# Kernel tuning notes

Hardware: AMD Instinct MI355X
Metric: run time of the kernel (lower is better)

## Reference

```python
import jax, jax.numpy as jnp
import numpy as np

B, D, KM1 = 8192, 256, 64  # batch, feature dim (no bias), num_classes-1
NC = KM1 + 1


def setup_inputs() -> dict:
    key = jax.random.key(0)
    k1, k2, k3 = jax.random.split(key, 3)
    features = jax.random.normal(k1, (B, D), dtype=jnp.float32)
    y = jax.random.randint(k2, (B,), 0, NC)
    mu = jax.random.normal(k3, (D, KM1), dtype=jnp.float32) * 0.001
    Sigma = jnp.broadcast_to(jnp.eye(D, dtype=jnp.float32), (KM1, D, D)).copy()
    return {"features": features, "y": y, "mu": mu, "Sigma": Sigma, "loss_type": 1}


def _b_ky(nc):
    # (nc, nc-1) stick-breaking selector matrix
    return 1.0 - jnp.pad(jnp.eye(nc)[..., :-2], [(0, 0), (1, 0)]).cumsum(-1)


def reference(features, y, mu, Sigma, loss_type):
    x = features                      # use_bias=False -> pad is a no-op
    logits = x @ mu                   # (B, K-1)
    bky = _b_ky(NC)                   # (K, K-1)
    y1h = jax.nn.one_hot(y, NC)       # (B, K)
    if loss_type == 0:
        full = jnp.pad(logits, [(0, 0), (0, 1)]) - jax.nn.softplus(logits) @ bky.T
        return -jnp.sum(full * y1h, -1)
    else:
        # psi_k = sqrt(x^T (Sigma_k + mu_k mu_k^T) x) = sqrt(x^T Sigma_k x + (x.mu_k)^2)
        xSx = jnp.einsum('bd,kde,be->bk', x, Sigma, x)   # (B, K-1)
        psi = jnp.sqrt(xSx + logits * logits)
        b = y1h @ bky                 # (B, K-1)
        kappa = y1h[..., :-1] - b / 2
        return -jnp.sum(logits * kappa + b * (psi / 2 - jax.nn.softplus(psi)), -1)
```

## Files before the change

### kernel.cpp

```cpp
#include <hip/hip_runtime.h>

typedef __attribute__((ext_vector_type(8))) short bf16x8;
typedef __attribute__((ext_vector_type(4))) float f32x4;

#define B_N 8192
#define D_N 256
#define K_N 64

__device__ __forceinline__ unsigned short bf16_rne(float f) {
  unsigned u = __builtin_bit_cast(unsigned, f);
  u += 0x7fffu + ((u >> 16) & 1u);
  return (unsigned short)(u >> 16);
}
__device__ __forceinline__ float bf16_f32(unsigned short h) {
  return __builtin_bit_cast(float, (unsigned)h << 16);
}

__device__ __forceinline__ void gload_lds16(const void* g, void* l) {
  __builtin_amdgcn_global_load_lds(
      (const __attribute__((address_space(1))) unsigned int*)g,
      (__attribute__((address_space(3))) unsigned int*)l, 16, 0, 0);
}

__global__ void convert_kernel(const float* __restrict__ src,
                               ushort* __restrict__ hi, ushort* __restrict__ lo,
                               int n4) {
  int idx = blockIdx.x * blockDim.x + threadIdx.x;
  int stride = gridDim.x * blockDim.x;
  for (int i = idx; i < n4; i += stride) {
    float4 v = ((const float4*)src)[i];
    ushort4 h, l;
    h.x = bf16_rne(v.x); l.x = bf16_rne(v.x - bf16_f32(h.x));
    h.y = bf16_rne(v.y); l.y = bf16_rne(v.y - bf16_f32(h.y));
    h.z = bf16_rne(v.z); l.z = bf16_rne(v.z - bf16_f32(h.z));
    h.w = bf16_rne(v.w); l.w = bf16_rne(v.w - bf16_f32(h.w));
    ((ushort4*)hi)[i] = h;
    ((ushort4*)lo)[i] = l;
  }
}

__global__ void convert_T_kernel(const float* __restrict__ Sigma,
                                 ushort* __restrict__ Th,
                                 ushort* __restrict__ Tl) {
  const int dtab[10] = {0, 0, 0, 0, 1, 1, 1, 2, 2, 3};
  const int etab[10] = {0, 1, 2, 3, 1, 2, 3, 2, 3, 3};
  const int k = blockIdx.x;
  const int dblk = dtab[blockIdx.y], eblk = etab[blockIdx.y];
  const float wgt = (dblk == eblk) ? 0.5f : 1.0f;
  const int tid = threadIdx.x;
  const int dl = tid >> 2;
  const int el0 = (tid & 3) * 16;
  const int d = dblk * 64 + dl;
  const size_t rowbase = ((size_t)k * D_N + d) * D_N + eblk * 64 + el0;
  const float* Srow = Sigma + rowbase;
  const float* Scol = Sigma + ((size_t)k * D_N + eblk * 64 + el0) * D_N + d;
  ushort h[16], l[16];
#pragma unroll
  for (int i = 0; i < 16; ++i) {
    const float t = (Srow[i] + Scol[(size_t)i * D_N]) * wgt;
    h[i] = bf16_rne(t);
    l[i] = bf16_rne(t - bf16_f32(h[i]));
  }
  *(uint4*)(Th + rowbase) = *(uint4*)&h[0];
  *(uint4*)(Th + rowbase + 8) = *(uint4*)&h[8];
  *(uint4*)(Tl + rowbase) = *(uint4*)&l[0];
  *(uint4*)(Tl + rowbase + 8) = *(uint4*)&l[8];
}

__global__ __launch_bounds__(256, 4) void xsx_tri2_kernel(
    const float* __restrict__ X,
    const ushort* __restrict__ Xh, const ushort* __restrict__ Xl,
    const ushort* __restrict__ Th, const ushort* __restrict__ Tl,
    float* __restrict__ part) {
  __shared__ __align__(16) ushort A_h[128][32];
  __shared__ __align__(16) ushort A_l[128][32];
  __shared__ __align__(16) ushort B_h[2][64][32];
  __shared__ __align__(16) ushort B_l[2][64][32];

  const int tid = threadIdx.x;
  const int lane = tid & 63;
  const int wid = tid >> 6;
  const int lr = lane & 15;
  const int lk = lane >> 4;

  const int bid = blockIdx.x;
  const int xcd = bid & 7;
  const int r = bid >> 3;
  const int qd = r >> 8;
  const int kp = (r >> 6) & 3;
  const int bg = r & 63;
  const int kk0 = xcd * 8 + kp * 2;
  const int bbase = bg * 128;

  const int srow = lane >> 2;
  const int sc = ((lane & 3) ^ ((lane >> 3) & 3)) * 8;
  const int rdc = (lk ^ ((lr >> 1) & 3)) * 8;

  f32x4 acc[2][2][4];
#pragma unroll
  for (int kp2 = 0; kp2 < 2; ++kp2)
#pragma unroll
    for (int mi = 0; mi < 2; ++mi)
#pragma unroll
      for (int ni = 0; ni < 4; ++ni)
        acc[kp2][mi][ni] = (f32x4){0.f, 0.f, 0.f, 0.f};

  const size_t a0 = (size_t)(bbase + wid * 32 + srow) * D_N + sc;
  const size_t bK0 = (size_t)kk0 * (D_N * D_N) +
                     (size_t)(qd * 64 + wid * 16 + srow) * D_N + sc;
  const size_t bK1 = bK0 + (size_t)(D_N * D_N);

  const int nch = 2 * (4 - qd);
  for (int c = 0; c < nch; ++c) {
    const int e0 = qd * 64 + c * 32;
    __syncthreads();
    gload_lds16(Xh + a0 + e0, &A_h[wid * 32][0]);
    gload_lds16(Xh + a0 + (size_t)16 * D_N + e0, &A_h[wid * 32 + 16][0]);
    gload_lds16(Xl + a0 + e0, &A_l[wid * 32][0]);
    gload_lds16(Xl + a0 + (size_t)16 * D_N + e0, &A_l[wid * 32 + 16][0]);
    gload_lds16(Th + bK0 + e0, &B_h[0][wid * 16][0]);
    gload_lds16(Tl + bK0 + e0, &B_l[0][wid * 16][0]);
    gload_lds16(Th + bK1 + e0, &B_h[1][wid * 16][0]);
    gload_lds16(Tl + bK1 + e0, &B_l[1][wid * 16][0]);
    __syncthreads();

    bf16x8 ah[2], al[2];
#pragma unroll
    for (int mi = 0; mi < 2; ++mi) {
      ah[mi] = *(const bf16x8*)&A_h[wid * 32 + mi * 16 + lr][rdc];
      al[mi] = *(const bf16x8*)&A_l[wid * 32 + mi * 16 + lr][rdc];
    }
#pragma unroll
    for (int kp2 = 0; kp2 < 2; ++kp2) {
#pragma unroll
      for (int ni = 0; ni < 4; ++ni) {
        const bf16x8 bh = *(const bf16x8*)&B_h[kp2][ni * 16 + lr][rdc];
        const bf16x8 bl = *(const bf16x8*)&B_l[kp2][ni * 16 + lr][rdc];
#pragma unroll
        for (int mi = 0; mi < 2; ++mi)
          acc[kp2][mi][ni] = __builtin_amdgcn_mfma_f32_16x16x32_bf16(
              ah[mi], bh, acc[kp2][mi][ni], 0, 0, 0);
#pragma unroll
        for (int mi = 0; mi < 2; ++mi)
          acc[kp2][mi][ni] = __builtin_amdgcn_mfma_f32_16x16x32_bf16(
              al[mi], bh, acc[kp2][mi][ni], 0, 0, 0);
#pragma unroll
        for (int mi = 0; mi < 2; ++mi)
          acc[kp2][mi][ni] = __builtin_amdgcn_mfma_f32_16x16x32_bf16(
              ah[mi], bl, acc[kp2][mi][ni], 0, 0, 0);
      }
    }
  }

#pragma unroll
  for (int kp2 = 0; kp2 < 2; ++kp2) {
#pragma unroll
    for (int mi = 0; mi < 2; ++mi) {
#pragma unroll
      for (int jj = 0; jj < 4; ++jj) {
        const int brow = bbase + wid * 32 + mi * 16 + lk * 4 + jj;
        const float* xr = X + (size_t)brow * D_N + qd * 64 + lr;
        float p = 0.f;
#pragma unroll
        for (int ni = 0; ni < 4; ++ni)
          p = fmaf(acc[kp2][mi][ni][jj], xr[ni * 16], p);
        p += __shfl_xor(p, 1);
        p += __shfl_xor(p, 2);
        p += __shfl_xor(p, 4);
        p += __shfl_xor(p, 8);
        if (lr == 0) part[((size_t)brow * K_N + kk0 + kp2) * 4 + qd] = p;
      }
    }
  }
}

__global__ __launch_bounds__(512, 2) void xsx_fallback(
    const float* __restrict__ X, const float* __restrict__ Sigma,
    float* __restrict__ xsx) {
  constexpr int BM = 128, KT = 32;
  __shared__ __align__(16) ushort Ah[BM][KT];
  __shared__ __align__(16) ushort Al[BM][KT];
  __shared__ __align__(16) ushort Bh[D_N][KT];
  __shared__ __align__(16) ushort Bl[D_N][KT];
  __shared__ float red[4][BM];

  const int tid = threadIdx.x;
  const int lane = tid & 63;
  const int wid = tid >> 6;
  const int wm = wid >> 2;
  const int wn = wid & 3;
  const int lr = lane & 15;
  const int lk = lane >> 4;

  const int b0 = blockIdx.x * BM;
  const int kk = blockIdx.y;
  const size_t soff = (size_t)kk * D_N * D_N;

  f32x4 acc[4][4];
#pragma unroll
  for (int mi = 0; mi < 4; ++mi)
#pragma unroll
    for (int ni = 0; ni < 4; ++ni) acc[mi][ni] = (f32x4){0.f, 0.f, 0.f, 0.f};

  for (int ec = 0; ec < D_N / KT; ++ec) {
    const int e0 = ec * KT;
    __syncthreads();
#pragma unroll
    for (int r = 0; r < 2; ++r) {
      const int i = tid + 512 * r;
      const int row = i >> 3, c4 = (i & 7) * 4;
      const float4 v = *(const float4*)(X + (size_t)(b0 + row) * D_N + e0 + c4);
      ushort4 h, l;
      h.x = bf16_rne(v.x); l.x = bf16_rne(v.x - bf16_f32(h.x));
      h.y = bf16_rne(v.y); l.y = bf16_rne(v.y - bf16_f32(h.y));
      h.z = bf16_rne(v.z); l.z = bf16_rne(v.z - bf16_f32(h.z));
      h.w = bf16_rne(v.w); l.w = bf16_rne(v.w - bf16_f32(h.w));
      *(ushort4*)&Ah[row][c4] = h;
      *(ushort4*)&Al[row][c4] = l;
    }
#pragma unroll
    for (int r = 0; r < 4; ++r) {
      const int i = tid + 512 * r;
      const int d = i >> 3, c4 = (i & 7) * 4;
      const float4 v = *(const float4*)(Sigma + soff + (size_t)d * D_N + e0 + c4);
      ushort4 h, l;
      h.x = bf16_rne(v.x); l.x = bf16_rne(v.x - bf16_f32(h.x));
      h.y = bf16_rne(v.y); l.y = bf16_rne(v.y - bf16_f32(h.y));
      h.z = bf16_rne(v.z); l.z = bf16_rne(v.z - bf16_f32(h.z));
      h.w = bf16_rne(v.w); l.w = bf16_rne(v.w - bf16_f32(h.w));
      *(ushort4*)&Bh[d][c4] = h;
      *(ushort4*)&Bl[d][c4] = l;
    }
    __syncthreads();

    bf16x8 ah[4], al[4];
#pragma unroll
    for (int mi = 0; mi < 4; ++mi) {
      ah[mi] = *(const bf16x8*)&Ah[wm * 64 + mi * 16 + lr][lk * 8];
      al[mi] = *(const bf16x8*)&Al[wm * 64 + mi * 16 + lr][lk * 8];
    }
#pragma unroll
    for (int ni = 0; ni < 4; ++ni) {
      const bf16x8 bh = *(const bf16x8*)&Bh[wn * 64 + ni * 16 + lr][lk * 8];
      const bf16x8 bl = *(const bf16x8*)&Bl[wn * 64 + ni * 16 + lr][lk * 8];
#pragma unroll
      for (int mi = 0; mi < 4; ++mi) {
        acc[mi][ni] = __builtin_amdgcn_mfma_f32_16x16x32_bf16(ah[mi], bh, acc[mi][ni], 0, 0, 0);
        acc[mi][ni] = __builtin_amdgcn_mfma_f32_16x16x32_bf16(al[mi], bh, acc[mi][ni], 0, 0, 0);
        acc[mi][ni] = __builtin_amdgcn_mfma_f32_16x16x32_bf16(ah[mi], bl, acc[mi][ni], 0, 0, 0);
      }
    }
  }

  float p[4][4];
#pragma unroll
  for (int mi = 0; mi < 4; ++mi)
#pragma unroll
    for (int jj = 0; jj < 4; ++jj) p[mi][jj] = 0.f;
#pragma unroll
  for (int mi = 0; mi < 4; ++mi) {
#pragma unroll
    for (int jj = 0; jj < 4; ++jj) {
      const int brow = b0 + wm * 64 + mi * 16 + lk * 4 + jj;
      const float* xr = X + (size_t)brow * D_N + wn * 64 + lr;
#pragma unroll
      for (int ni = 0; ni < 4; ++ni)
        p[mi][jj] = fmaf(acc[mi][ni][jj], xr[ni * 16], p[mi][jj]);
    }
  }
#pragma unroll
  for (int mi = 0; mi < 4; ++mi)
#pragma unroll
    for (int jj = 0; jj < 4; ++jj) {
      float v = p[mi][jj];
      v += __shfl_xor(v, 1);
      v += __shfl_xor(v, 2);
      v += __shfl_xor(v, 4);
      v += __shfl_xor(v, 8);
      p[mi][jj] = v;
    }
  if (lr == 0) {
#pragma unroll
    for (int mi = 0; mi < 4; ++mi)
#pragma unroll
      for (int jj = 0; jj < 4; ++jj)
        red[wn][wm * 64 + mi * 16 + lk * 4 + jj] = p[mi][jj];
  }
  __syncthreads();
  if (tid < BM) {
    const float s = red[0][tid] + red[1][tid] + red[2][tid] + red[3][tid];
    xsx[(size_t)(b0 + tid) * K_N + kk] = s;
  }
}

__global__ __launch_bounds__(256) void loss_kernel(
    const float* __restrict__ X, const int* __restrict__ y,
    const float* __restrict__ mu, const int* __restrict__ loss_type,
    const float* __restrict__ xsx, float* __restrict__ out, int nparts) {
  __shared__ float mu_s[D_N * K_N];
  __shared__ float x_s[4][D_N];
  const int tid = threadIdx.x;
  const int wid = tid >> 6;
  const int lane = tid & 63;
  const int b = blockIdx.x * 4 + wid;

  for (int i = tid; i < D_N * K_N / 4; i += 256)
    ((float4*)mu_s)[i] = ((const float4*)mu)[i];
  ((float4*)&x_s[wid][0])[lane] = ((const float4*)(X + (size_t)b * D_N))[lane];
  __syncthreads();

  const int yb = y[b];
  const int lt = loss_type[0];

  float logit = 0.f;
#pragma unroll 8
  for (int d = 0; d < D_N; ++d)
    logit = fmaf(x_s[wid][d], mu_s[d * K_N + lane], logit);

  float term;
  if (lt == 1) {
    float xv;
    if (nparts == 4) {
      const float4 pv = *(const float4*)(xsx + ((size_t)b * K_N + lane) * 4);
      xv = ((pv.x + pv.y) + pv.z) + pv.w;
    } else {
      xv = xsx[(size_t)b * K_N + lane];
    }
    const float psi = sqrtf(fmaxf(xv + logit * logit, 0.f));
    const float bk = (lane <= yb) ? 1.f : 0.f;
    const float kap = ((lane == yb) ? 1.f : 0.f) - 0.5f * bk;
    term = logit * kap + bk * (-0.5f * psi - log1pf(expf(-psi)));
  } else {
    const float sp = (logit > 0.f) ? (logit + log1pf(expf(-logit)))
                                   : log1pf(expf(logit));
    term = ((lane == yb) ? logit : 0.f) - ((lane <= yb) ? sp : 0.f);
  }
#pragma unroll
  for (int s = 1; s < 64; s <<= 1) term += __shfl_xor(term, s);
  if (lane == 0) out[b] = -term;
}

extern "C" void kernel_launch(void* const* d_in, const int* in_sizes, int n_in,
                              void* d_out, int out_size, void* d_ws, size_t ws_size,
                              hipStream_t stream) {
  const float* X = (const float*)d_in[0];
  const int* y = (const int*)d_in[1];
  const float* mu = (const float*)d_in[2];
  const float* Sigma = (const float*)d_in[3];
  const int* lt = (const int*)d_in[4];
  float* out = (float*)d_out;

  const size_t XN = (size_t)B_N * D_N;
  const size_t SN = (size_t)K_N * D_N * D_N;
  const size_t xh_off = 0;
  const size_t xl_off = xh_off + XN * 2;
  const size_t th_off = xl_off + XN * 2;
  const size_t tl_off = th_off + SN * 2;
  const size_t part_off = tl_off + SN * 2;
  const size_t need = part_off + (size_t)B_N * K_N * 4 * 4;

  char* w = (char*)d_ws;
  if (ws_size >= need) {
    ushort* Xh = (ushort*)(w + xh_off);
    ushort* Xl = (ushort*)(w + xl_off);
    ushort* Th = (ushort*)(w + th_off);
    ushort* Tl = (ushort*)(w + tl_off);
    float* part = (float*)(w + part_off);
    hipLaunchKernelGGL(convert_kernel, dim3(1024), dim3(256), 0, stream,
                       X, Xh, Xl, (int)(XN / 4));
    hipLaunchKernelGGL(convert_T_kernel, dim3(64, 10), dim3(256), 0, stream,
                       Sigma, Th, Tl);
    hipLaunchKernelGGL(xsx_tri2_kernel, dim3(8192), dim3(256), 0, stream,
                       X, Xh, Xl, Th, Tl, part);
    hipLaunchKernelGGL(loss_kernel, dim3(B_N / 4), dim3(256), 0, stream,
                       X, y, mu, lt, part, out, 4);
  } else {
    float* xsx = (float*)w;
    hipLaunchKernelGGL(xsx_fallback, dim3(B_N / 128, K_N), dim3(512), 0, stream,
                       X, Sigma, xsx);
    hipLaunchKernelGGL(loss_kernel, dim3(B_N / 4), dim3(256), 0, stream,
                       X, y, mu, lt, xsx, out, 1);
  }
}
```

Baseline: 202.1 us.

## Split xSx blocks to one class each and batch loss kernel rows per block

The xSx MFMA kernel now handles a single class k per block instead of two, which halves the B-tile shared memory and accumulators and doubles the grid to 16384 blocks. This gives more parallelism and lower register pressure, but each X tile is loaded twice as often. The loss kernel now processes 32 rows per block instead of 4. That cuts the number of times the 64KB mu matrix is copied into shared memory per block, but enlarges shared memory use and runs a serial loop of 8 rows per wave.

```diff
diff --git a/kernel.cpp b/kernel.cpp
--- a/kernel.cpp
+++ b/kernel.cpp
@@ -67,15 +67,15 @@
   *(uint4*)(Tl + rowbase + 8) = *(uint4*)&l[8];
 }
 
-__global__ __launch_bounds__(256, 4) void xsx_tri2_kernel(
+__global__ __launch_bounds__(256, 4) void xsx_tri3_kernel(
     const float* __restrict__ X,
     const ushort* __restrict__ Xh, const ushort* __restrict__ Xl,
     const ushort* __restrict__ Th, const ushort* __restrict__ Tl,
     float* __restrict__ part) {
   __shared__ __align__(16) ushort A_h[128][32];
   __shared__ __align__(16) ushort A_l[128][32];
-  __shared__ __align__(16) ushort B_h[2][64][32];
-  __shared__ __align__(16) ushort B_l[2][64][32];
+  __shared__ __align__(16) ushort B_h[64][32];
+  __shared__ __align__(16) ushort B_l[64][32];
 
   const int tid = threadIdx.x;
   const int lane = tid & 63;
@@ -86,29 +86,25 @@
   const int bid = blockIdx.x;
   const int xcd = bid & 7;
   const int r = bid >> 3;
-  const int qd = r >> 8;
-  const int kp = (r >> 6) & 3;
-  const int bg = r & 63;
-  const int kk0 = xcd * 8 + kp * 2;
+  const int qd = r >> 9;
+  const int s = r & 511;
+  const int kk = xcd * 8 + (s & 7);
+  const int bg = s >> 3;
   const int bbase = bg * 128;
 
   const int srow = lane >> 2;
   const int sc = ((lane & 3) ^ ((lane >> 3) & 3)) * 8;
   const int rdc = (lk ^ ((lr >> 1) & 3)) * 8;
 
-  f32x4 acc[2][2][4];
-#pragma unroll
-  for (int kp2 = 0; kp2 < 2; ++kp2)
-#pragma unroll
-    for (int mi = 0; mi < 2; ++mi)
-#pragma unroll
-      for (int ni = 0; ni < 4; ++ni)
-        acc[kp2][mi][ni] = (f32x4){0.f, 0.f, 0.f, 0.f};
+  f32x4 acc[2][4];
+#pragma unroll
+  for (int mi = 0; mi < 2; ++mi)
+#pragma unroll
+    for (int ni = 0; ni < 4; ++ni) acc[mi][ni] = (f32x4){0.f, 0.f, 0.f, 0.f};
 
   const size_t a0 = (size_t)(bbase + wid * 32 + srow) * D_N + sc;
-  const size_t bK0 = (size_t)kk0 * (D_N * D_N) +
-                     (size_t)(qd * 64 + wid * 16 + srow) * D_N + sc;
-  const size_t bK1 = bK0 + (size_t)(D_N * D_N);
+  const size_t bK = (size_t)kk * (D_N * D_N) +
+                    (size_t)(qd * 64 + wid * 16 + srow) * D_N + sc;
 
   const int nch = 2 * (4 - qd);
   for (int c = 0; c < nch; ++c) {
@@ -118,10 +114,8 @@
     gload_lds16(Xh + a0 + (size_t)16 * D_N + e0, &A_h[wid * 32 + 16][0]);
     gload_lds16(Xl + a0 + e0, &A_l[wid * 32][0]);
     gload_lds16(Xl + a0 + (size_t)16 * D_N + e0, &A_l[wid * 32 + 16][0]);
-    gload_lds16(Th + bK0 + e0, &B_h[0][wid * 16][0]);
-    gload_lds16(Tl + bK0 + e0, &B_l[0][wid * 16][0]);
-    gload_lds16(Th + bK1 + e0, &B_h[1][wid * 16][0]);
-    gload_lds16(Tl + bK1 + e0, &B_l[1][wid * 16][0]);
+    gload_lds16(Th + bK + e0, &B_h[wid * 16][0]);
+    gload_lds16(Tl + bK + e0, &B_l[wid * 16][0]);
     __syncthreads();
 
     bf16x8 ah[2], al[2];
@@ -131,45 +125,38 @@
       al[mi] = *(const bf16x8*)&A_l[wid * 32 + mi * 16 + lr][rdc];
     }
 #pragma unroll
-    for (int kp2 = 0; kp2 < 2; ++kp2) {
-#pragma unroll
-      for (int ni = 0; ni < 4; ++ni) {
-        const bf16x8 bh = *(const bf16x8*)&B_h[kp2][ni * 16 + lr][rdc];
-        const bf16x8 bl = *(const bf16x8*)&B_l[kp2][ni * 16 + lr][rdc];
-#pragma unroll
-        for (int mi = 0; mi < 2; ++mi)
-          acc[kp2][mi][ni] = __builtin_amdgcn_mfma_f32_16x16x32_bf16(
-              ah[mi], bh, acc[kp2][mi][ni], 0, 0, 0);
-#pragma unroll
-        for (int mi = 0; mi < 2; ++mi)
-          acc[kp2][mi][ni] = __builtin_amdgcn_mfma_f32_16x16x32_bf16(
-              al[mi], bh, acc[kp2][mi][ni], 0, 0, 0);
-#pragma unroll
-        for (int mi = 0; mi < 2; ++mi)
-          acc[kp2][mi][ni] = __builtin_amdgcn_mfma_f32_16x16x32_bf16(
-              ah[mi], bl, acc[kp2][mi][ni], 0, 0, 0);
-      }
-    }
-  }
-
-#pragma unroll
-  for (int kp2 = 0; kp2 < 2; ++kp2) {
-#pragma unroll
-    for (int mi = 0; mi < 2; ++mi) {
-#pragma unroll
-      for (int jj = 0; jj < 4; ++jj) {
-        const int brow = bbase + wid * 32 + mi * 16 + lk * 4 + jj;
-        const float* xr = X + (size_t)brow * D_N + qd * 64 + lr;
-        float p = 0.f;
-#pragma unroll
-        for (int ni = 0; ni < 4; ++ni)
-          p = fmaf(acc[kp2][mi][ni][jj], xr[ni * 16], p);
-        p += __shfl_xor(p, 1);
-        p += __shfl_xor(p, 2);
-        p += __shfl_xor(p, 4);
-        p += __shfl_xor(p, 8);
-        if (lr == 0) part[((size_t)brow * K_N + kk0 + kp2) * 4 + qd] = p;
-      }
+    for (int ni = 0; ni < 4; ++ni) {
+      const bf16x8 bh = *(const bf16x8*)&B_h[ni * 16 + lr][rdc];
+      const bf16x8 bl = *(const bf16x8*)&B_l[ni * 16 + lr][rdc];
+#pragma unroll
+      for (int mi = 0; mi < 2; ++mi)
+        acc[mi][ni] = __builtin_amdgcn_mfma_f32_16x16x32_bf16(
+            ah[mi], bh, acc[mi][ni], 0, 0, 0);
+#pragma unroll
+      for (int mi = 0; mi < 2; ++mi)
+        acc[mi][ni] = __builtin_amdgcn_mfma_f32_16x16x32_bf16(
+            al[mi], bh, acc[mi][ni], 0, 0, 0);
+#pragma unroll
+      for (int mi = 0; mi < 2; ++mi)
+        acc[mi][ni] = __builtin_amdgcn_mfma_f32_16x16x32_bf16(
+            ah[mi], bl, acc[mi][ni], 0, 0, 0);
+    }
+  }
+
+#pragma unroll
+  for (int mi = 0; mi < 2; ++mi) {
+#pragma unroll
+    for (int jj = 0; jj < 4; ++jj) {
+      const int brow = bbase + wid * 32 + mi * 16 + lk * 4 + jj;
+      const float* xr = X + (size_t)brow * D_N + qd * 64 + lr;
+      float p = 0.f;
+#pragma unroll
+      for (int ni = 0; ni < 4; ++ni) p = fmaf(acc[mi][ni][jj], xr[ni * 16], p);
+      p += __shfl_xor(p, 1);
+      p += __shfl_xor(p, 2);
+      p += __shfl_xor(p, 4);
+      p += __shfl_xor(p, 8);
+      if (lr == 0) part[((size_t)brow * K_N + kk) * 4 + qd] = p;
     }
   }
 }
@@ -293,51 +280,61 @@
   }
 }
 
-__global__ __launch_bounds__(256) void loss_kernel(
+__global__ __launch_bounds__(256) void loss_kernel2(
     const float* __restrict__ X, const int* __restrict__ y,
     const float* __restrict__ mu, const int* __restrict__ loss_type,
     const float* __restrict__ xsx, float* __restrict__ out, int nparts) {
   __shared__ float mu_s[D_N * K_N];
-  __shared__ float x_s[4][D_N];
+  __shared__ float x_s[32][D_N];
   const int tid = threadIdx.x;
   const int wid = tid >> 6;
   const int lane = tid & 63;
-  const int b = blockIdx.x * 4 + wid;
+  const int brow0 = blockIdx.x * 32;
 
   for (int i = tid; i < D_N * K_N / 4; i += 256)
     ((float4*)mu_s)[i] = ((const float4*)mu)[i];
-  ((float4*)&x_s[wid][0])[lane] = ((const float4*)(X + (size_t)b * D_N))[lane];
+#pragma unroll
+  for (int i = 0; i < 8; ++i) {
+    const int row = (tid >> 6) * 8 + i;
+    ((float4*)&x_s[row][0])[lane] =
+        ((const float4*)(X + (size_t)(brow0 + row) * D_N))[lane];
+  }
   __syncthreads();
 
-  const int yb = y[b];
   const int lt = loss_type[0];
 
-  float logit = 0.f;
+  for (int i = 0; i < 8; ++i) {
+    const int row = wid * 8 + i;
+    const int b = brow0 + row;
+    const int yb = y[b];
+
+    float logit = 0.f;
 #pragma unroll 8
-  for (int d = 0; d < D_N; ++d)
-    logit = fmaf(x_s[wid][d], mu_s[d * K_N + lane], logit);
-
-  float term;
-  if (lt == 1) {
-    float xv;
-    if (nparts == 4) {
-      const float4 pv = *(const float4*)(xsx + ((size_t)b * K_N + lane) * 4);
-      xv = ((pv.x + pv.y) + pv.z) + pv.w;
+    for (int d = 0; d < D_N; ++d)
+      logit = fmaf(x_s[row][d], mu_s[d * K_N + lane], logit);
+
+    float term;
+    if (lt == 1) {
+      float xv;
+      if (nparts == 4) {
+        const float4 pv = *(const float4*)(xsx + ((size_t)b * K_N + lane) * 4);
+        xv = ((pv.x + pv.y) + pv.z) + pv.w;
+      } else {
+        xv = xsx[(size_t)b * K_N + lane];
+      }
+      const float psi = sqrtf(fmaxf(xv + logit * logit, 0.f));
+      const float bk = (lane <= yb) ? 1.f : 0.f;
+      const float kap = ((lane == yb) ? 1.f : 0.f) - 0.5f * bk;
+      term = logit * kap + bk * (-0.5f * psi - log1pf(expf(-psi)));
     } else {
-      xv = xsx[(size_t)b * K_N + lane];
-    }
-    const float psi = sqrtf(fmaxf(xv + logit * logit, 0.f));
-    const float bk = (lane <= yb) ? 1.f : 0.f;
-    const float kap = ((lane == yb) ? 1.f : 0.f) - 0.5f * bk;
-    term = logit * kap + bk * (-0.5f * psi - log1pf(expf(-psi)));
-  } else {
-    const float sp = (logit > 0.f) ? (logit + log1pf(expf(-logit)))
-                                   : log1pf(expf(logit));
-    term = ((lane == yb) ? logit : 0.f) - ((lane <= yb) ? sp : 0.f);
-  }
-#pragma unroll
-  for (int s = 1; s < 64; s <<= 1) term += __shfl_xor(term, s);
-  if (lane == 0) out[b] = -term;
+      const float sp = (logit > 0.f) ? (logit + log1pf(expf(-logit)))
+                                     : log1pf(expf(logit));
+      term = ((lane == yb) ? logit : 0.f) - ((lane <= yb) ? sp : 0.f);
+    }
+#pragma unroll
+    for (int s = 1; s < 64; s <<= 1) term += __shfl_xor(term, s);
+    if (lane == 0) out[b] = -term;
+  }
 }
 
 extern "C" void kernel_launch(void* const* d_in, const int* in_sizes, int n_in,
@@ -370,15 +367,15 @@
                        X, Xh, Xl, (int)(XN / 4));
     hipLaunchKernelGGL(convert_T_kernel, dim3(64, 10), dim3(256), 0, stream,
                        Sigma, Th, Tl);
-    hipLaunchKernelGGL(xsx_tri2_kernel, dim3(8192), dim3(256), 0, stream,
+    hipLaunchKernelGGL(xsx_tri3_kernel, dim3(16384), dim3(256), 0, stream,
                        X, Xh, Xl, Th, Tl, part);
-    hipLaunchKernelGGL(loss_kernel, dim3(B_N / 4), dim3(256), 0, stream,
+    hipLaunchKernelGGL(loss_kernel2, dim3(B_N / 32), dim3(256), 0, stream,
                        X, y, mu, lt, part, out, 4);
   } else {
     float* xsx = (float*)w;
     hipLaunchKernelGGL(xsx_fallback, dim3(B_N / 128, K_N), dim3(512), 0, stream,
                        X, Sigma, xsx);
-    hipLaunchKernelGGL(loss_kernel, dim3(B_N / 4), dim3(256), 0, stream,
+    hipLaunchKernelGGL(loss_kernel2, dim3(B_N / 32), dim3(256), 0, stream,
                        X, y, mu, lt, xsx, out, 1);
   }
 }
```

Measured after the change: 200.4 us. No clear change (-0.8%).
